# Performance work log

Hardware: AMD Instinct MI355X
Metric: run time of the kernel (lower is better)

The kernel has to match this reference:

```python
import jax, jax.numpy as jnp
import numpy as np

N_NODES = 65536   # sli * node = 512 * 128
N_EDGES = 524288  # avg degree 8
SLI, NODE = 512, 128
SLOPE = 0.01      # nn.LeakyReLU default negative_slope


def leaky_relu(v):
    return jnp.where(v >= 0, v, SLOPE * v)


def graph_conv(h, src, dst, W, b):
    """DGL GraphConv with norm='both': D_in^{-1/2} A D_out^{-1/2} h W + b, then LeakyReLU."""
    ones = jnp.ones(src.shape[0], dtype=h.dtype)
    out_deg = jnp.clip(jax.ops.segment_sum(ones, src, num_segments=N_NODES), 1.0)
    in_deg = jnp.clip(jax.ops.segment_sum(ones, dst, num_segments=N_NODES), 1.0)
    h = h * jax.lax.rsqrt(out_deg)[:, None]                     # src-side norm
    agg = jax.ops.segment_sum(h[src], dst, num_segments=N_NODES)  # gather + scatter-add
    agg = agg * jax.lax.rsqrt(in_deg)[:, None]                  # dst-side norm
    return leaky_relu(agg @ W + b)


def graphsage(x, src, dst, W, b):
    # x: [sli, C, node] -> [sli*node, C] -> GraphConv -> [sli, F, node]
    sli, C, node = x.shape
    h = x.transpose(0, 2, 1).reshape(-1, C)
    h = graph_conv(h, src, dst, W, b)
    return h.reshape(sli, node, -1).transpose(0, 2, 1)


def conv1x1(x, W, b):
    # pointwise Conv1d: x [S, Cin, N], W [Cout, Cin] -> [S, Cout, N]
    return jnp.einsum('scn,oc->son', x, W) + b[None, :, None]


def setup_inputs() -> dict:
    key = jax.random.key(0)
    ks = jax.random.split(key, 16)
    d = {
        'x': jax.random.normal(ks[0], (SLI, 128, NODE), dtype=jnp.float32),
        'edge_src': jax.random.randint(ks[1], (N_EDGES,), 0, N_NODES, dtype=jnp.int32),
        'edge_dst': jax.random.randint(ks[2], (N_EDGES,), 0, N_NODES, dtype=jnp.int32),
        'W_head': jax.random.normal(ks[3], (128, 128), dtype=jnp.float32) * 0.05,
        'b_head': jnp.zeros((128,), dtype=jnp.float32),
        'W_res0': jax.random.normal(ks[4], (128, 128), dtype=jnp.float32) * 0.05,
        'b_res0': jnp.zeros((128,), dtype=jnp.float32),
        'W_res1': jax.random.normal(ks[5], (128, 128), dtype=jnp.float32) * 0.05,
        'b_res1': jnp.zeros((128,), dtype=jnp.float32),
        'W_res2': jax.random.normal(ks[6], (128, 128), dtype=jnp.float32) * 0.05,
        'b_res2': jnp.zeros((128,), dtype=jnp.float32),
        'W_fusion': jax.random.normal(ks[7], (256, 512), dtype=jnp.float32) * 0.05,
        'b_fusion': jnp.zeros((256,), dtype=jnp.float32),
        'W_p1': jax.random.normal(ks[8], (256, 768), dtype=jnp.float32) * 0.05,
        'b_p1': jnp.zeros((256,), dtype=jnp.float32),
        'W_p2': jax.random.normal(ks[9], (64, 256), dtype=jnp.float32) * 0.05,
        'b_p2': jnp.zeros((64,), dtype=jnp.float32),
        'W_p3': jax.random.normal(ks[10], (2, 64), dtype=jnp.float32) * 0.05,
        'b_p3': jnp.zeros((2,), dtype=jnp.float32),
    }
    return d


def reference(x, edge_src, edge_dst, W_head, b_head, W_res0, b_res0, W_res1, b_res1,
              W_res2, b_res2, W_fusion, b_fusion, W_p1, b_p1, W_p2, b_p2, W_p3, b_p3):
    h = graphsage(x, edge_src, edge_dst, W_head, b_head)   # [S, 128, N]
    states = [h]
    for W, b in ((W_res0, b_res0), (W_res1, b_res1), (W_res2, b_res2)):
        h = graphsage(h, edge_src, edge_dst, W, b) + h     # residual
        states.append(h)
    state = jnp.concatenate(states, axis=1)                # [S, 512, N]
    fused = conv1x1(state, W_fusion, b_fusion)             # [S, 256, N]
    global_state = jnp.max(fused, axis=2, keepdims=True)   # [S, 256, 1]
    global_state = jnp.broadcast_to(global_state, (state.shape[0], 256, state.shape[2]))
    state = jnp.concatenate([global_state, state], axis=1) # [S, 768, N]
    y = leaky_relu(conv1x1(state, W_p1, b_p1))
    y = leaky_relu(conv1x1(y, W_p2, b_p2))
    return conv1x1(y, W_p3, b_p3)                          # [S, 2, N]
```

## Files before the change

kernel.cpp:

```cpp
#include <hip/hip_runtime.h>

#define NN 65536
#define NE 524288
#define SLOPE 0.01f

typedef unsigned short us;
typedef __attribute__((ext_vector_type(8))) short short8;
typedef __attribute__((ext_vector_type(4))) float f32x4;

__device__ __forceinline__ float leaky(float v) { return v >= 0.f ? v : SLOPE * v; }
__device__ __forceinline__ float b2f(us u) { return __uint_as_float(((unsigned)u) << 16); }
__device__ __forceinline__ us f2b(float f) {
  unsigned u = __float_as_uint(f);
  u += 0x7fffu + ((u >> 16) & 1u);
  return (us)(u >> 16);
}
__device__ __forceinline__ void split2(float v, us& hi, us& lo) {
  hi = f2b(v);
  lo = f2b(v - b2f(hi));
}

__device__ __forceinline__ void gload16(const void* g, void* l) {
  __builtin_amdgcn_global_load_lds(
      (const __attribute__((address_space(1))) unsigned int*)g,
      (__attribute__((address_space(3))) unsigned int*)l, 16, 0, 0);
}

__global__ void zero_ints(int* __restrict__ p, int n) {
  int i = blockIdx.x * blockDim.x + threadIdx.x;
  if (i < n) p[i] = 0;
}

__global__ void deg_count(const int* __restrict__ src, const int* __restrict__ dst,
                          int* __restrict__ cout, int* __restrict__ cin) {
  int e = blockIdx.x * blockDim.x + threadIdx.x;
  if (e < NE) {
    atomicAdd(&cout[src[e]], 1);
    atomicAdd(&cin[dst[e]], 1);
  }
}

__global__ void rs_kernel(const int* __restrict__ cout, const int* __restrict__ cin,
                          float* __restrict__ rs_out, float* __restrict__ rs_in) {
  int n = blockIdx.x * blockDim.x + threadIdx.x;
  if (n < NN) {
    rs_out[n] = rsqrtf((float)(cout[n] > 0 ? cout[n] : 1));
    rs_in[n]  = rsqrtf((float)(cin[n]  > 0 ? cin[n]  : 1));
  }
}

__global__ __launch_bounds__(1024) void scan_kernel(const int* __restrict__ cnt,
                                                    int* __restrict__ row_ptr) {
  __shared__ int part[1024];
  int t = threadIdx.x;
  int base = t * 64;
  int s = 0;
  for (int i = 0; i < 64; ++i) s += cnt[base + i];
  part[t] = s;
  __syncthreads();
  for (int d = 1; d < 1024; d <<= 1) {
    int v = (t >= d) ? part[t - d] : 0;
    __syncthreads();
    part[t] += v;
    __syncthreads();
  }
  int run = part[t] - s;
  for (int i = 0; i < 64; ++i) { row_ptr[base + i] = run; run += cnt[base + i]; }
  if (t == 1023) row_ptr[NN] = run;
}

__global__ void csr_fill(const int* __restrict__ src, const int* __restrict__ dst,
                         const int* __restrict__ row_ptr, int* __restrict__ cursor,
                         int* __restrict__ csr) {
  int e = blockIdx.x * blockDim.x + threadIdx.x;
  if (e < NE) {
    int d = dst[e];
    int pos = atomicAdd(&cursor[d], 1);
    csr[row_ptr[d] + pos] = src[e];
  }
}

__global__ __launch_bounds__(256) void transpose_x(const float* __restrict__ x,
                                                   us* __restrict__ h0h,
                                                   us* __restrict__ h0l) {
  __shared__ float tile[128][68];
  int s  = blockIdx.x >> 1;
  int vh = (blockIdx.x & 1) * 64;
  const float* xs = x + (size_t)s * 16384;
  int t = threadIdx.x;
  int v4 = t & 15, c0 = t >> 4;
  for (int p = 0; p < 8; ++p) {
    int c = c0 + p * 16;
    float4 val = *(const float4*)(xs + (size_t)c * 128 + vh + v4 * 4);
    *(float4*)&tile[c][v4 * 4] = val;
  }
  __syncthreads();
  int c4 = t & 31, v0 = t >> 5;
  for (int p = 0; p < 8; ++p) {
    int v = v0 + p * 8;
    float o[4];
    o[0] = tile[c4 * 4 + 0][v];
    o[1] = tile[c4 * 4 + 1][v];
    o[2] = tile[c4 * 4 + 2][v];
    o[3] = tile[c4 * 4 + 3][v];
    us hh[4], ll[4];
#pragma unroll
    for (int j = 0; j < 4; ++j) split2(o[j], hh[j], ll[j]);
    size_t off = (size_t)(s * 128 + vh + v) * 128 + c4 * 4;
    uint2 wh = make_uint2((unsigned)hh[0] | ((unsigned)hh[1] << 16),
                          (unsigned)hh[2] | ((unsigned)hh[3] << 16));
    uint2 wl = make_uint2((unsigned)ll[0] | ((unsigned)ll[1] << 16),
                          (unsigned)ll[2] | ((unsigned)ll[3] << 16));
    *(uint2*)(h0h + off) = wh;
    *(uint2*)(h0l + off) = wl;
  }
}

__global__ void wsplit(const float* __restrict__ src, us* __restrict__ bh,
                       us* __restrict__ bl, int N, int K, int ld, int koff) {
  int idx = blockIdx.x * 256 + threadIdx.x;
  if (idx >= N * K) return;
  int n = idx / K, k = idx - n * K;
  float v = src[(size_t)n * ld + koff + k];
  us hi, lo; split2(v, hi, lo);
  bh[idx] = hi; bl[idx] = lo;
}

__global__ void wsplit_t(const float* __restrict__ src, us* __restrict__ bh,
                         us* __restrict__ bl, int N, int K, int ld) {
  int idx = blockIdx.x * 256 + threadIdx.x;
  if (idx >= N * K) return;
  int n = idx / K, k = idx - n * K;
  float v = src[(size_t)k * ld + n];
  us hi, lo; split2(v, hi, lo);
  bh[idx] = hi; bl[idx] = lo;
}

__global__ __launch_bounds__(256) void aggregate(
    const us* __restrict__ hh, const us* __restrict__ hl, int lda,
    const int* __restrict__ row_ptr, const int* __restrict__ csr,
    const float* __restrict__ rs_out, const float* __restrict__ rs_in,
    us* __restrict__ aggh, us* __restrict__ aggl) {
  const int lane = threadIdx.x & 63;
  const int n = blockIdx.x * 4 + (threadIdx.x >> 6);
  const us* base = ((lane < 32) ? hh : hl) + (size_t)(lane & 31) * 4;
  const int b = row_ptr[n], e = row_ptr[n + 1];
  float a0 = 0.f, a1 = 0.f, a2 = 0.f, a3 = 0.f;
  int i = b;
  for (; i + 2 <= e; i += 2) {
    int s0 = csr[i], s1 = csr[i + 1];
    uint2 v0 = *(const uint2*)(base + (size_t)s0 * lda);
    uint2 v1 = *(const uint2*)(base + (size_t)s1 * lda);
    float w0 = rs_out[s0], w1 = rs_out[s1];
    a0 = fmaf(w0, __uint_as_float(v0.x << 16), a0);
    a1 = fmaf(w0, __uint_as_float(v0.x & 0xffff0000u), a1);
    a2 = fmaf(w0, __uint_as_float(v0.y << 16), a2);
    a3 = fmaf(w0, __uint_as_float(v0.y & 0xffff0000u), a3);
    a0 = fmaf(w1, __uint_as_float(v1.x << 16), a0);
    a1 = fmaf(w1, __uint_as_float(v1.x & 0xffff0000u), a1);
    a2 = fmaf(w1, __uint_as_float(v1.y << 16), a2);
    a3 = fmaf(w1, __uint_as_float(v1.y & 0xffff0000u), a3);
  }
  if (i < e) {
    int s0 = csr[i];
    uint2 v0 = *(const uint2*)(base + (size_t)s0 * lda);
    float w0 = rs_out[s0];
    a0 = fmaf(w0, __uint_as_float(v0.x << 16), a0);
    a1 = fmaf(w0, __uint_as_float(v0.x & 0xffff0000u), a1);
    a2 = fmaf(w0, __uint_as_float(v0.y << 16), a2);
    a3 = fmaf(w0, __uint_as_float(v0.y & 0xffff0000u), a3);
  }
  a0 += __shfl_xor(a0, 32);
  a1 += __shfl_xor(a1, 32);
  a2 += __shfl_xor(a2, 32);
  a3 += __shfl_xor(a3, 32);
  const float ri = rs_in[n];
  a0 *= ri; a1 *= ri; a2 *= ri; a3 *= ri;
  us h[4], l[4];
  split2(a0, h[0], l[0]); split2(a1, h[1], l[1]);
  split2(a2, h[2], l[2]); split2(a3, h[3], l[3]);
  size_t o = (size_t)n * 128 + (size_t)(lane & 31) * 4;
  if (lane < 32) {
    uint2 wv = make_uint2((unsigned)h[0] | ((unsigned)h[1] << 16),
                          (unsigned)h[2] | ((unsigned)h[3] << 16));
    *(uint2*)(aggh + o) = wv;
  } else {
    uint2 wv = make_uint2((unsigned)l[0] | ((unsigned)l[1] << 16),
                          (unsigned)l[2] | ((unsigned)l[3] << 16));
    *(uint2*)(aggl + o) = wv;
  }
}

template<int KTOT, int NF, int MODE, int NSPLIT>
__global__ __launch_bounds__(512, 4) void mgemm(
    const us* __restrict__ Ah, const us* __restrict__ Al, int lda,
    const us* __restrict__ Bh, const us* __restrict__ Bl,
    const float* __restrict__ bias,
    float* __restrict__ outf, us* __restrict__ outh, us* __restrict__ outl,
    int ldo, int colOff,
    const us* __restrict__ prevh, const us* __restrict__ prevl,
    const float* __restrict__ gcon) {
  constexpr int BN  = NF * 64;
  constexpr int BCH = BN * 4;
  constexpr int BSH = (NF == 2) ? 7 : 6;
  constexpr int NT  = KTOT / 32;

  __shared__ __align__(16) us sAh[2][4][128][8];
  __shared__ __align__(16) us sAl[2][4][128][8];
  __shared__ __align__(16) us sBh[2][4][BN][8];
  __shared__ __align__(16) us sBl[2][4][BN][8];

  const int t = threadIdx.x;
  int mb, nb;
  if constexpr (NSPLIT == 2) {
    int lid = (blockIdx.x & 7) * ((int)gridDim.x >> 3) + (blockIdx.x >> 3);
    mb = lid >> 1; nb = lid & 1;
  } else {
    mb = blockIdx.x; nb = 0;
  }
  const int mbase = mb * 128;
  const int nbase = nb * BN;

  const int akb = t >> 7, ar = t & 127;
  const us* gAh = Ah + (size_t)(mbase + ar) * lda + akb * 8;
  const us* gAl = Al + (size_t)(mbase + ar) * lda + akb * 8;
  const bool bact = (t < BCH);
  const int bkb = (t >> BSH) & 3, br = t & (BN - 1);
  const us* gBh = Bh + (size_t)(nbase + br) * KTOT + bkb * 8;
  const us* gBl = Bl + (size_t)(nbase + br) * KTOT + bkb * 8;

  const int lane = t & 63, wv = t >> 6;
  const int wm = wv & 1, wn = wv >> 1;
  const int l15 = lane & 15, lkb = lane >> 4;

  f32x4 acc[4][NF];
#pragma unroll
  for (int i = 0; i < 4; ++i)
#pragma unroll
    for (int j = 0; j < NF; ++j)
#pragma unroll
      for (int e = 0; e < 4; ++e) acc[i][j][e] = 0.f;

  auto stage = [&](int buf, int k0) {
    gload16(gAh + k0, &sAh[buf][akb][ar][0]);
    gload16(gAl + k0, &sAl[buf][akb][ar][0]);
    if (bact) {
      gload16(gBh + k0, &sBh[buf][bkb][br][0]);
      gload16(gBl + k0, &sBl[buf][bkb][br][0]);
    }
  };

  stage(0, 0);
  __syncthreads();
  int cur = 0;

  for (int kt = 0; kt < NT; ++kt) {
    if (kt + 1 < NT) stage(cur ^ 1, (kt + 1) * 32);

    short8 ah[4], al[4], bh[NF], bl[NF];
#pragma unroll
    for (int fm = 0; fm < 4; ++fm) {
      ah[fm] = *(const short8*)&sAh[cur][lkb][wm * 64 + fm * 16 + l15][0];
      al[fm] = *(const short8*)&sAl[cur][lkb][wm * 64 + fm * 16 + l15][0];
    }
#pragma unroll
    for (int fn = 0; fn < NF; ++fn) {
      bh[fn] = *(const short8*)&sBh[cur][lkb][wn * (NF * 16) + fn * 16 + l15][0];
      bl[fn] = *(const short8*)&sBl[cur][lkb][wn * (NF * 16) + fn * 16 + l15][0];
    }
#pragma unroll
    for (int fm = 0; fm < 4; ++fm)
#pragma unroll
      for (int fn = 0; fn < NF; ++fn)
        acc[fm][fn] = __builtin_amdgcn_mfma_f32_16x16x32_bf16(ah[fm], bh[fn], acc[fm][fn], 0, 0, 0);
#pragma unroll
    for (int fm = 0; fm < 4; ++fm)
#pragma unroll
      for (int fn = 0; fn < NF; ++fn)
        acc[fm][fn] = __builtin_amdgcn_mfma_f32_16x16x32_bf16(al[fm], bh[fn], acc[fm][fn], 0, 0, 0);
#pragma unroll
    for (int fm = 0; fm < 4; ++fm)
#pragma unroll
      for (int fn = 0; fn < NF; ++fn)
        acc[fm][fn] = __builtin_amdgcn_mfma_f32_16x16x32_bf16(ah[fm], bl[fn], acc[fm][fn], 0, 0, 0);

    __syncthreads();
    cur ^= 1;
  }

  if constexpr (MODE == 0 || MODE == 1 || MODE == 3) {
    const float* gc = (MODE == 3) ? (gcon + (size_t)mb * 256 + nbase) : nullptr;
#pragma unroll
    for (int fm = 0; fm < 4; ++fm)
#pragma unroll
      for (int fn = 0; fn < NF; ++fn) {
        const int col = wn * (NF * 16) + fn * 16 + l15;
        float bb = bias[nbase + col];
        if constexpr (MODE == 3) bb += gc[col];
#pragma unroll
        for (int r = 0; r < 4; ++r) {
          const int row = mbase + wm * 64 + fm * 16 + lkb * 4 + r;
          float v = leaky(acc[fm][fn][r] + bb);
          const size_t off = (size_t)row * ldo + colOff + nbase + col;
          if constexpr (MODE == 1) v += b2f(prevh[off - 128]) + b2f(prevl[off - 128]);
          us hi, lo; split2(v, hi, lo);
          outh[off] = hi;
          outl[off] = lo;
        }
      }
  } else if constexpr (MODE == 2) {
    __shared__ float red[2][128];
#pragma unroll
    for (int fn = 0; fn < NF; ++fn) {
      float m = acc[0][fn][0];
#pragma unroll
      for (int fm = 0; fm < 4; ++fm)
#pragma unroll
        for (int r = 0; r < 4; ++r) m = fmaxf(m, acc[fm][fn][r]);
      m = fmaxf(m, __shfl_xor(m, 16));
      m = fmaxf(m, __shfl_xor(m, 32));
      if (lane < 16) red[wm][wn * (NF * 16) + fn * 16 + l15] = m;
    }
    __syncthreads();
    if (t < 128)
      outf[(size_t)mb * 256 + nbase + t] = fmaxf(red[0][t], red[1][t]) + bias[nbase + t];
  } else {
#pragma unroll
    for (int fm = 0; fm < 4; ++fm) {
      const int col = wn * 16 + l15;
      const float bb = bias[col];
#pragma unroll
      for (int r = 0; r < 4; ++r) {
        const int row = mbase + wm * 64 + fm * 16 + lkb * 4 + r;
        outf[(size_t)row * 64 + col] = leaky(acc[fm][0][r] + bb);
      }
    }
  }
}

__global__ void gcon_kernel(const float* __restrict__ gmax, const float* __restrict__ Wp1,
                            float* __restrict__ gcon) {
  __shared__ float g[256];
  int s = blockIdx.x, o = threadIdx.x;
  g[o] = gmax[(size_t)s * 256 + o];
  __syncthreads();
  float acc = 0.f;
  const float* wr = Wp1 + (size_t)o * 768;
#pragma unroll 8
  for (int c = 0; c < 256; ++c) acc += g[c] * wr[c];
  gcon[(size_t)s * 256 + o] = acc;
}

__global__ void p3_kernel(const float* __restrict__ y2, const float* __restrict__ W,
                          const float* __restrict__ b, float* __restrict__ out) {
  __shared__ float w0[64], w1[64];
  int t = threadIdx.x;
  if (t < 64) { w0[t] = W[t]; w1[t] = W[64 + t]; }
  __syncthreads();
  int n = blockIdx.x * 256 + t;
  const float* row = y2 + (size_t)n * 64;
  float a0 = b[0], a1 = b[1];
#pragma unroll
  for (int j = 0; j < 64; j += 4) {
    float4 v = *(const float4*)(row + j);
    a0 += v.x * w0[j] + v.y * w0[j + 1] + v.z * w0[j + 2] + v.w * w0[j + 3];
    a1 += v.x * w1[j] + v.y * w1[j + 1] + v.z * w1[j + 2] + v.w * w1[j + 3];
  }
  int s = n >> 7, vv = n & 127;
  out[((size_t)s * 2 + 0) * 128 + vv] = a0;
  out[((size_t)s * 2 + 1) * 128 + vv] = a1;
}

extern "C" void kernel_launch(void* const* d_in, const int* in_sizes, int n_in,
                              void* d_out, int out_size, void* d_ws, size_t ws_size,
                              hipStream_t stream) {
  const float* x        = (const float*)d_in[0];
  const int*   esrc     = (const int*)d_in[1];
  const int*   edst     = (const int*)d_in[2];
  const float* W_head   = (const float*)d_in[3];
  const float* b_head   = (const float*)d_in[4];
  const float* W_res[3] = {(const float*)d_in[5], (const float*)d_in[7], (const float*)d_in[9]};
  const float* b_res[3] = {(const float*)d_in[6], (const float*)d_in[8], (const float*)d_in[10]};
  const float* W_fusion = (const float*)d_in[11];
  const float* b_fusion = (const float*)d_in[12];
  const float* W_p1     = (const float*)d_in[13];
  const float* b_p1     = (const float*)d_in[14];
  const float* W_p2     = (const float*)d_in[15];
  const float* b_p2     = (const float*)d_in[16];
  const float* W_p3     = (const float*)d_in[17];
  const float* b_p3     = (const float*)d_in[18];
  float* outp = (float*)d_out;

  char* w = (char*)d_ws;
  size_t off = 0;
  auto alloc = [&](size_t bytes) { char* p = w + off; off += (bytes + 255) & ~(size_t)255; return p; };

  us* states_h = (us*)alloc((size_t)NN * 512 * 2);
  us* states_l = (us*)alloc((size_t)NN * 512 * 2);
  char* regionA = alloc((size_t)NN * 128 * 2 * 4);
  us* h0h  = (us*)regionA;
  us* h0l  = (us*)(regionA + (size_t)NN * 128 * 2);
  us* aggh = (us*)(regionA + (size_t)NN * 128 * 4);
  us* aggl = (us*)(regionA + (size_t)NN * 128 * 6);
  us* y1h  = (us*)regionA;
  us* y1l  = (us*)(regionA + (size_t)NN * 256 * 2);
  float* y2 = (float*)states_h;

  float* gmax   = (float*)alloc(512 * 256 * 4);
  float* gcon   = (float*)alloc(512 * 256 * 4);
  float* rs_out = (float*)alloc((size_t)NN * 4);
  float* rs_in  = (float*)alloc((size_t)NN * 4);
  us* cWh[4]; us* cWl[4];
  for (int l = 0; l < 4; ++l) { cWh[l] = (us*)alloc(128 * 128 * 2); cWl[l] = (us*)alloc(128 * 128 * 2); }
  us* fWh  = (us*)alloc(256 * 512 * 2);
  us* fWl  = (us*)alloc(256 * 512 * 2);
  us* p1Wh = (us*)alloc(256 * 512 * 2);
  us* p1Wl = (us*)alloc(256 * 512 * 2);
  us* p2Wh = (us*)alloc(64 * 256 * 2);
  us* p2Wl = (us*)alloc(64 * 256 * 2);
  int* cnt_out = (int*)alloc((size_t)NN * 4);
  int* cnt_in  = (int*)alloc((size_t)NN * 4);
  int* cursor  = (int*)alloc((size_t)NN * 4);
  int* row_ptr = (int*)alloc(((size_t)NN + 1) * 4);
  int* csr     = (int*)alloc((size_t)NE * 4);

  zero_ints<<<(3 * NN + 255) / 256, 256, 0, stream>>>(cnt_out, 3 * NN);
  deg_count<<<NE / 256, 256, 0, stream>>>(esrc, edst, cnt_out, cnt_in);
  rs_kernel<<<NN / 256, 256, 0, stream>>>(cnt_out, cnt_in, rs_out, rs_in);
  scan_kernel<<<1, 1024, 0, stream>>>(cnt_in, row_ptr);
  csr_fill<<<NE / 256, 256, 0, stream>>>(esrc, edst, row_ptr, cursor, csr);

  transpose_x<<<1024, 256, 0, stream>>>(x, h0h, h0l);
  const float* cW[4] = {W_head, W_res[0], W_res[1], W_res[2]};
  for (int l = 0; l < 4; ++l)
    wsplit_t<<<64, 256, 0, stream>>>(cW[l], cWh[l], cWl[l], 128, 128, 128);
  wsplit<<<512, 256, 0, stream>>>(W_fusion, fWh, fWl, 256, 512, 512, 0);
  wsplit<<<512, 256, 0, stream>>>(W_p1, p1Wh, p1Wl, 256, 512, 768, 256);
  wsplit<<<64, 256, 0, stream>>>(W_p2, p2Wh, p2Wl, 64, 256, 256, 0);

  const float* cB[4] = {b_head, b_res[0], b_res[1], b_res[2]};
  aggregate<<<NN / 4, 256, 0, stream>>>(h0h, h0l, 128, row_ptr, csr, rs_out, rs_in, aggh, aggl);
  mgemm<128, 2, 0, 1><<<512, 512, 0, stream>>>(aggh, aggl, 128, cWh[0], cWl[0], cB[0],
                                               nullptr, states_h, states_l, 512, 0,
                                               nullptr, nullptr, nullptr);
  for (int l = 1; l <= 3; ++l) {
    aggregate<<<NN / 4, 256, 0, stream>>>(states_h + (size_t)(l - 1) * 128,
                                          states_l + (size_t)(l - 1) * 128, 512,
                                          row_ptr, csr, rs_out, rs_in, aggh, aggl);
    mgemm<128, 2, 1, 1><<<512, 512, 0, stream>>>(aggh, aggl, 128, cWh[l], cWl[l], cB[l],
                                                 nullptr, states_h, states_l, 512, l * 128,
                                                 states_h, states_l, nullptr);
  }
  mgemm<512, 2, 2, 2><<<1024, 512, 0, stream>>>(states_h, states_l, 512, fWh, fWl, b_fusion,
                                                gmax, nullptr, nullptr, 0, 0,
                                                nullptr, nullptr, nullptr);
  gcon_kernel<<<512, 256, 0, stream>>>(gmax, W_p1, gcon);
  mgemm<512, 2, 3, 2><<<1024, 512, 0, stream>>>(states_h, states_l, 512, p1Wh, p1Wl, b_p1,
                                                nullptr, y1h, y1l, 256, 0,
                                                nullptr, nullptr, gcon);
  mgemm<256, 1, 4, 1><<<512, 512, 0, stream>>>(y1h, y1l, 256, p2Wh, p2Wl, b_p2,
                                               y2, nullptr, nullptr, 0, 0,
                                               nullptr, nullptr, nullptr);
  p3_kernel<<<NN / 256, 256, 0, stream>>>(y2, W_p3, b_p3, outp);
}
```

Measured before the change: 638.0 us.

## Deepen GEMM prefetch with explicit vmcnt waits and unroll aggregation loop by four

The GEMM mainloop is restructured so every thread issues an equal share of the async global-to-LDS loads from precomputed pointers. Both buffers are prefetched ahead, and fine-grained s_waitcnt vmcnt waits with raw barriers and setprio around the MFMAs replace the per-iteration __syncthreads. The intent is to keep two tiles in flight and overlap loads with matrix math. Separately, the neighbor-gather loop in aggregation is unrolled to four edges per iteration to raise memory-level parallelism. The hand-coded vmcnt counts depend on LPT and the loop assumes an even tile count, so any mismatch would break correctness.

Result: no change. 628.4 us (-1.5%).

```diff
diff --git a/kernel.cpp b/kernel.cpp
--- a/kernel.cpp
+++ b/kernel.cpp
@@ -147,11 +147,13 @@
   const int b = row_ptr[n], e = row_ptr[n + 1];
   float a0 = 0.f, a1 = 0.f, a2 = 0.f, a3 = 0.f;
   int i = b;
-  for (; i + 2 <= e; i += 2) {
-    int s0 = csr[i], s1 = csr[i + 1];
+  for (; i + 4 <= e; i += 4) {
+    int s0 = csr[i], s1 = csr[i + 1], s2 = csr[i + 2], s3 = csr[i + 3];
     uint2 v0 = *(const uint2*)(base + (size_t)s0 * lda);
     uint2 v1 = *(const uint2*)(base + (size_t)s1 * lda);
-    float w0 = rs_out[s0], w1 = rs_out[s1];
+    uint2 v2 = *(const uint2*)(base + (size_t)s2 * lda);
+    uint2 v3 = *(const uint2*)(base + (size_t)s3 * lda);
+    float w0 = rs_out[s0], w1 = rs_out[s1], w2 = rs_out[s2], w3 = rs_out[s3];
     a0 = fmaf(w0, __uint_as_float(v0.x << 16), a0);
     a1 = fmaf(w0, __uint_as_float(v0.x & 0xffff0000u), a1);
     a2 = fmaf(w0, __uint_as_float(v0.y << 16), a2);
@@ -160,8 +162,16 @@
     a1 = fmaf(w1, __uint_as_float(v1.x & 0xffff0000u), a1);
     a2 = fmaf(w1, __uint_as_float(v1.y << 16), a2);
     a3 = fmaf(w1, __uint_as_float(v1.y & 0xffff0000u), a3);
-  }
-  if (i < e) {
+    a0 = fmaf(w2, __uint_as_float(v2.x << 16), a0);
+    a1 = fmaf(w2, __uint_as_float(v2.x & 0xffff0000u), a1);
+    a2 = fmaf(w2, __uint_as_float(v2.y << 16), a2);
+    a3 = fmaf(w2, __uint_as_float(v2.y & 0xffff0000u), a3);
+    a0 = fmaf(w3, __uint_as_float(v3.x << 16), a0);
+    a1 = fmaf(w3, __uint_as_float(v3.x & 0xffff0000u), a1);
+    a2 = fmaf(w3, __uint_as_float(v3.y << 16), a2);
+    a3 = fmaf(w3, __uint_as_float(v3.y & 0xffff0000u), a3);
+  }
+  for (; i < e; ++i) {
     int s0 = csr[i];
     uint2 v0 = *(const uint2*)(base + (size_t)s0 * lda);
     float w0 = rs_out[s0];
@@ -201,9 +211,9 @@
     const us* __restrict__ prevh, const us* __restrict__ prevl,
     const float* __restrict__ gcon) {
   constexpr int BN  = NF * 64;
-  constexpr int BCH = BN * 4;
-  constexpr int BSH = (NF == 2) ? 7 : 6;
+  constexpr int LB  = (NF == 2) ? 7 : 6;
   constexpr int NT  = KTOT / 32;
+  constexpr int LPT = 2 + (BN * 8) / 512;
 
   __shared__ __align__(16) us sAh[2][4][128][8];
   __shared__ __align__(16) us sAl[2][4][128][8];
@@ -221,16 +231,40 @@
   const int mbase = mb * 128;
   const int nbase = nb * BN;
 
-  const int akb = t >> 7, ar = t & 127;
-  const us* gAh = Ah + (size_t)(mbase + ar) * lda + akb * 8;
-  const us* gAl = Al + (size_t)(mbase + ar) * lda + akb * 8;
-  const bool bact = (t < BCH);
-  const int bkb = (t >> BSH) & 3, br = t & (BN - 1);
-  const us* gBh = Bh + (size_t)(nbase + br) * KTOT + bkb * 8;
-  const us* gBl = Bl + (size_t)(nbase + br) * KTOT + bkb * 8;
-
-  const int lane = t & 63, wv = t >> 6;
-  const int wm = wv & 1, wn = wv >> 1;
+  const us* gp[LPT];
+  us* lp0[LPT];
+  us* lp1[LPT];
+#pragma unroll
+  for (int i = 0; i < LPT; ++i) {
+    int id = i * 512 + t;
+    if (id < 512) {
+      int row = id & 127, kb = id >> 7;
+      gp[i]  = Ah + (size_t)(mbase + row) * lda + kb * 8;
+      lp0[i] = &sAh[0][kb][row][0];
+      lp1[i] = &sAh[1][kb][row][0];
+    } else if (id < 1024) {
+      int c = id - 512;
+      int row = c & 127, kb = c >> 7;
+      gp[i]  = Al + (size_t)(mbase + row) * lda + kb * 8;
+      lp0[i] = &sAl[0][kb][row][0];
+      lp1[i] = &sAl[1][kb][row][0];
+    } else if (id < 1024 + BN * 4) {
+      int c = id - 1024;
+      int row = c & (BN - 1), kb = c >> LB;
+      gp[i]  = Bh + (size_t)(nbase + row) * KTOT + kb * 8;
+      lp0[i] = &sBh[0][kb][row][0];
+      lp1[i] = &sBh[1][kb][row][0];
+    } else {
+      int c = id - 1024 - BN * 4;
+      int row = c & (BN - 1), kb = c >> LB;
+      gp[i]  = Bl + (size_t)(nbase + row) * KTOT + kb * 8;
+      lp0[i] = &sBl[0][kb][row][0];
+      lp1[i] = &sBl[1][kb][row][0];
+    }
+  }
+
+  const int lane = t & 63, wvi = t >> 6;
+  const int wm = wvi & 1, wn = wvi >> 1;
   const int l15 = lane & 15, lkb = lane >> 4;
 
   f32x4 acc[4][NF];
@@ -241,33 +275,37 @@
 #pragma unroll
       for (int e = 0; e < 4; ++e) acc[i][j][e] = 0.f;
 
-  auto stage = [&](int buf, int k0) {
-    gload16(gAh + k0, &sAh[buf][akb][ar][0]);
-    gload16(gAl + k0, &sAl[buf][akb][ar][0]);
-    if (bact) {
-      gload16(gBh + k0, &sBh[buf][bkb][br][0]);
-      gload16(gBl + k0, &sBl[buf][bkb][br][0]);
+  auto stageb = [&](us* const* lp, int k0) {
+#pragma unroll
+    for (int i = 0; i < LPT; ++i) gload16(gp[i] + k0, lp[i]);
+  };
+  auto waitL = [&]() {
+    if constexpr (LPT == 4) asm volatile("s_waitcnt vmcnt(4)" ::: "memory");
+    else                    asm volatile("s_waitcnt vmcnt(3)" ::: "memory");
+    __builtin_amdgcn_sched_barrier(0);
+  };
+  auto wait0 = [&]() {
+    asm volatile("s_waitcnt vmcnt(0)" ::: "memory");
+    __builtin_amdgcn_sched_barrier(0);
+  };
+  auto bar = [&]() {
+    __builtin_amdgcn_s_barrier();
+    __builtin_amdgcn_sched_barrier(0);
+  };
+  auto kstep = [&](us (&bAh)[4][128][8], us (&bAl)[4][128][8],
+                   us (&bBh)[4][BN][8], us (&bBl)[4][BN][8]) {
+    short8 ah[4], al[4], bh[NF], bl[NF];
+#pragma unroll
+    for (int fm = 0; fm < 4; ++fm) {
+      ah[fm] = *(const short8*)&bAh[lkb][wm * 64 + fm * 16 + l15][0];
+      al[fm] = *(const short8*)&bAl[lkb][wm * 64 + fm * 16 + l15][0];
     }
-  };
-
-  stage(0, 0);
-  __syncthreads();
-  int cur = 0;
-
-  for (int kt = 0; kt < NT; ++kt) {
-    if (kt + 1 < NT) stage(cur ^ 1, (kt + 1) * 32);
-
-    short8 ah[4], al[4], bh[NF], bl[NF];
-#pragma unroll
-    for (int fm = 0; fm < 4; ++fm) {
-      ah[fm] = *(const short8*)&sAh[cur][lkb][wm * 64 + fm * 16 + l15][0];
-      al[fm] = *(const short8*)&sAl[cur][lkb][wm * 64 + fm * 16 + l15][0];
+#pragma unroll
+    for (int fn = 0; fn < NF; ++fn) {
+      bh[fn] = *(const short8*)&bBh[lkb][wn * (NF * 16) + fn * 16 + l15][0];
+      bl[fn] = *(const short8*)&bBl[lkb][wn * (NF * 16) + fn * 16 + l15][0];
     }
-#pragma unroll
-    for (int fn = 0; fn < NF; ++fn) {
-      bh[fn] = *(const short8*)&sBh[cur][lkb][wn * (NF * 16) + fn * 16 + l15][0];
-      bl[fn] = *(const short8*)&sBl[cur][lkb][wn * (NF * 16) + fn * 16 + l15][0];
-    }
+    __builtin_amdgcn_s_setprio(1);
 #pragma unroll
     for (int fm = 0; fm < 4; ++fm)
 #pragma unroll
@@ -283,9 +321,22 @@
 #pragma unroll
       for (int fn = 0; fn < NF; ++fn)
         acc[fm][fn] = __builtin_amdgcn_mfma_f32_16x16x32_bf16(ah[fm], bl[fn], acc[fm][fn], 0, 0, 0);
-
-    __syncthreads();
-    cur ^= 1;
+    __builtin_amdgcn_s_setprio(0);
+  };
+
+  stageb(lp0, 0);
+  stageb(lp1, 32);
+#pragma unroll 1
+  for (int kt = 0; kt < NT; kt += 2) {
+    waitL(); bar();
+    kstep(sAh[0], sAl[0], sBh[0], sBl[0]);
+    bar();
+    if (kt + 2 < NT) stageb(lp0, (kt + 2) * 32);
+    if (kt + 3 < NT) waitL(); else wait0();
+    bar();
+    kstep(sAh[1], sAl[1], sBh[1], sBl[1]);
+    bar();
+    if (kt + 3 < NT) stageb(lp1, (kt + 3) * 32);
   }
 
   if constexpr (MODE == 0 || MODE == 1 || MODE == 3) {
```
